# Performance work log

Measured on AMD Instinct MI355X. Metric: run time of the kernel, lower is better.

Reference implementation:

```python
import jax, jax.numpy as jnp
import numpy as np

BINS = 256

def _conv_x(t, k):
    # t: [N,1,H,W], k: [3] tap filter along width, 'same' padding
    return jax.lax.conv_general_dilated(t, k.reshape(1, 1, 1, 3), (1, 1), [(0, 0), (1, 1)])

def _conv_y(t, k):
    # t: [N,1,H,W], k: [3] tap filter along height, 'same' padding
    return jax.lax.conv_general_dilated(t, k.reshape(1, 1, 3, 1), (1, 1), [(1, 1), (0, 0)])

def calc_invCR(x):
    # Vectorized equivalent of the per-slice torch.histc loop:
    # 256-bin histogram over [-1,1] per (batch*channel) slice, Shannon entropy in bits / 8.
    n, _, h, w = x.shape
    res = h * w
    xf = x.reshape(n, res)
    valid = ((xf >= -1.0) & (xf <= 1.0)).astype(jnp.float32)
    # bin index; value exactly == max (1.0) falls into the last bin, matching torch.histc
    bins = jnp.clip(jnp.floor((xf + 1.0) * (BINS / 2.0)), 0, BINS - 1).astype(jnp.int32)
    counts = jnp.zeros((n, BINS), jnp.float32).at[jnp.arange(n)[:, None], bins].add(valid)
    p = counts / res
    ent = jnp.sum(jnp.where(p > 0, -p * jnp.log2(jnp.where(p > 0, p, 1.0)), 0.0))
    return ent / (8.0 * n)

def _forward(x, px, ux, cx, rx, py, uy, cy, ry):
    b, c, h, w = x.shape
    img = x.reshape(b * c, 1, h, w)
    cur = img
    xos, yos = [], []
    for lvl in range(5):
        xe, xo = cur[:, :, :, ::2], cur[:, :, :, 1::2]
        xo = xo - _conv_x(xe, px)
        xe = xe + _conv_x(xo, ux)
        xo = xo - _conv_x(xe, cx)
        xe = xe + _conv_x(xo, rx)
        ye, yo = xe[:, :, ::2, :], xe[:, :, 1::2, :]
        yo = yo - _conv_y(ye, py)
        if lvl < 2:
            ye = ye + _conv_y(yo, uy)
        # levels 3-5 in the source apply update_y to the (discarded) x?e tensor
        # (`x3e = x3e + self.update_y(x3o)`); that result is never used, so it is a
        # no-op for the output and is faithfully omitted here.
        yo = yo - _conv_y(ye, cy)
        ye = ye + _conv_y(yo, ry)
        xos.append(xo)
        yos.append(yo)
        cur = ye
    out = cur
    for xo, yo in zip(reversed(xos), reversed(yos)):
        out = jnp.concatenate((jnp.concatenate((out, yo), axis=2), xo), axis=3)
    deltas = jnp.fmod(out + 1.0, 2.0) - 1.0  # wrap residuals into [-1,1]
    loss1 = 255.0 * jnp.sqrt(jnp.mean(jnp.square(deltas)))
    loss0 = 255.0 * jnp.sqrt(jnp.mean(jnp.square(img)))
    invCR0 = calc_invCR(img)
    invCR1 = calc_invCR(deltas)
    return loss1, loss0, invCR0, invCR1

def setup_inputs() -> dict:
    key = jax.random.key(0)
    ks = jax.random.split(key, 9)
    inp = {"x": jax.random.uniform(ks[0], (32, 3, 512, 512), jnp.float32)}
    for i, name in enumerate(["px", "ux", "cx", "rx", "py", "uy", "cy", "ry"]):
        inp[name] = 0.25 * jax.random.normal(ks[i + 1], (3,), jnp.float32)
    return inp

def reference(x, px, ux, cx, rx, py, uy, cy, ry):
    return _forward(x, px, ux, cx, rx, py, uy, cy, ry)
```

## Files before the change

### kernel.cpp

```cpp
#include <hip/hip_runtime.h>
#include <math.h>

#define NIMG 96
#define NSLOT 1024
#define RES_INV (1.0f / 262144.0f)

__device__ __forceinline__ float wrap1(float v) {
  float t = v + 1.0f;
  return t - 2.0f * truncf(t * 0.5f) - 1.0f;
}
__device__ __forceinline__ int bin_fast(float v) {
  int b = (int)fmaf(v, 128.0f, 128.0f);
  return (b > 255) ? 255 : b;
}

template<int P, int SEGP, int USE_UY, int DO_IMG>
__global__ void __launch_bounds__(256) klift_fused(
    const float* __restrict__ src, float* __restrict__ ye_out,
    const float* __restrict__ kpx, const float* __restrict__ kux,
    const float* __restrict__ kcx, const float* __restrict__ krx,
    const float* __restrict__ kpy, const float* __restrict__ kuy,
    const float* __restrict__ kcy, const float* __restrict__ kry,
    double* __restrict__ partial,
    unsigned* __restrict__ hist_img, unsigned* __restrict__ hist_delta)
{
  constexpr int W2 = 64 * P;
  constexpr int H2 = W2;
  constexpr int H  = 2 * H2;
  constexpr int NP = SEGP + 8;
  constexpr int NR = 2 * NP;
  constexpr int NITER = NR / 4;
  __shared__ float tile[NR][W2];
  __shared__ unsigned shd[2][256];
  __shared__ unsigned shi[2][256];

  const int t = threadIdx.x, w = t >> 6, lane = t & 63;
  const int hsel = w >> 1;
  const int img = blockIdx.y;
  const int R0 = blockIdx.x * SEGP;
  const int base_in = 2 * R0 - 8;

  shd[0][t] = 0; shd[1][t] = 0;
  if (DO_IMG) { shi[0][t] = 0; shi[1][t] = 0; }
  __syncthreads();

  const float px0 = kpx[0], px1 = kpx[1], px2 = kpx[2];
  const float ux0 = kux[0], ux1 = kux[1], ux2 = kux[2];
  const float cx0 = kcx[0], cx1 = kcx[1], cx2 = kcx[2];
  const float rx0 = krx[0], rx1 = krx[1], rx2 = krx[2];
  const float py0 = kpy[0], py1 = kpy[1], py2 = kpy[2];
  const float uy0 = kuy[0], uy1 = kuy[1], uy2 = kuy[2];
  const float cy0 = kcy[0], cy1 = kcy[1], cy2 = kcy[2];
  const float ry0 = kry[0], ry1 = kry[1], ry2 = kry[2];

  const float* ip = src + (size_t)img * H * (2 * W2);
  float sqi = 0.f, sqd = 0.f;

  auto stepm = [&](float (&d)[P], float (&s)[P], float k0, float k1, float k2) {
    float L = __shfl_up(s[P - 1], 1); if (lane == 0) L = 0.f;
    float R = __shfl_down(s[0], 1);   if (lane == 63) R = 0.f;
    float prev = L;
#pragma unroll
    for (int j = 0; j < P; j++) {
      float nxt = (j == P - 1) ? R : s[(j + 1) < P ? (j + 1) : 0];
      d[j] = fmaf(k0, prev, fmaf(k1, s[j], fmaf(k2, nxt, d[j])));
      prev = s[j];
    }
  };
  auto ldrow = [&](int lr, float4& A, float4& B, bool chk) {
    const int gin = base_in + lr;
    if (!chk || ((unsigned)gin < (unsigned)H)) {
      const float* rp = ip + (size_t)gin * (2 * W2) + lane * (2 * P);
      if (P == 1) { float2 v = *(const float2*)rp; A.x = v.x; A.y = v.y; }
      else {
        A = *(const float4*)rp;
        if (P == 4) B = *(const float4*)(rp + 4);
      }
    } else {
      A = make_float4(0.f, 0.f, 0.f, 0.f);
      B = make_float4(0.f, 0.f, 0.f, 0.f);
    }
  };

  const int wcol = (P == 4) ? ((lane ^ ((lane >> 3) & 7)) * 4)
                 : (P == 2) ? (lane * 2) : lane;

  float4 cA = make_float4(0.f,0.f,0.f,0.f), cB = cA, nA = cA, nB = cA;
  ldrow(w, cA, cB, true);
#pragma unroll
  for (int i = 0; i < NITER; ++i) {
    const int lr = w + 4 * i;
    if (i + 1 < NITER)
      ldrow(lr + 4, nA, nB, (i + 1 < 2) || (i + 1 >= NITER - 2));
    const bool owned = (i >= 2) && (i < NITER - 2);
    float e[P], o[P];
    e[0] = cA.x; o[0] = cA.y;
    if (P >= 2) { e[P > 1 ? 1 : 0] = cA.z; o[P > 1 ? 1 : 0] = cA.w; }
    if (P == 4) {
      e[P > 2 ? 2 : 0] = cB.x; o[P > 2 ? 2 : 0] = cB.y;
      e[P > 3 ? 3 : 0] = cB.z; o[P > 3 ? 3 : 0] = cB.w;
    }
    if (DO_IMG && owned) {
#pragma unroll
      for (int j = 0; j < P; j++) {
        sqi += e[j] * e[j] + o[j] * o[j];
        atomicAdd(&shi[hsel][bin_fast(e[j])], 1u);
        atomicAdd(&shi[hsel][bin_fast(o[j])], 1u);
      }
    }
    stepm(o, e, -px0, -px1, -px2);
    stepm(e, o,  ux0,  ux1,  ux2);
    stepm(o, e, -cx0, -cx1, -cx2);
    stepm(e, o,  rx0,  rx1,  rx2);
    if (P == 4) {
      *(float4*)&tile[lr][wcol] =
          make_float4(e[0], e[P > 1 ? 1 : 0], e[P > 2 ? 2 : 0], e[P > 3 ? 3 : 0]);
    } else if (P == 2) {
      *(float2*)&tile[lr][wcol] = make_float2(e[0], e[P > 1 ? 1 : 0]);
    } else {
      tile[lr][wcol] = e[0];
    }
    if (owned) {
#pragma unroll
      for (int j = 0; j < P; j++) {
        float d = wrap1(o[j]);
        sqd += d * d;
        atomicAdd(&shd[hsel][bin_fast(d)], 1u);
      }
    }
    cA = nA; cB = nB;
  }
  __syncthreads();

  {
    constexpr int NSP = 256 / W2;
    constexpr int LEN = SEGP / NSP;
    constexpr int WIN = LEN + 8;
    const int col = t % W2;
    const int half = t / W2;
    const int q0 = half * LEN;
    int colr;
    if (P == 4) {
      const int ch = (col >> 2) ^ ((col >> 5) & 7);
      colr = (ch << 2) | (col & 3);
    } else colr = col;

    float ee[WIN], oo[WIN];
#pragma unroll
    for (int q = 0; q < WIN; ++q) {
      ee[q] = tile[2 * (q0 + q)][colr];
      oo[q] = tile[2 * (q0 + q) + 1][colr];
    }
#pragma unroll
    for (int q = 0; q < WIN; ++q) {
      float U = (q > 0) ? ee[q - 1] : 0.f;
      float D = (q < WIN - 1) ? ee[q + 1] : 0.f;
      oo[q] = fmaf(-py0, U, fmaf(-py1, ee[q], fmaf(-py2, D, oo[q])));
    }
    if (USE_UY) {
#pragma unroll
      for (int q = 0; q < WIN; ++q) {
        float U = (q > 0) ? oo[q - 1] : 0.f;
        float D = (q < WIN - 1) ? oo[q + 1] : 0.f;
        ee[q] = fmaf(uy0, U, fmaf(uy1, oo[q], fmaf(uy2, D, ee[q])));
      }
    }
#pragma unroll
    for (int q = 0; q < WIN; ++q) {
      float U = (q > 0) ? ee[q - 1] : 0.f;
      float D = (q < WIN - 1) ? ee[q + 1] : 0.f;
      oo[q] = fmaf(-cy0, U, fmaf(-cy1, ee[q], fmaf(-cy2, D, oo[q])));
    }
#pragma unroll
    for (int q = 0; q < WIN; ++q) {
      float U = (q > 0) ? oo[q - 1] : 0.f;
      float D = (q < WIN - 1) ? oo[q + 1] : 0.f;
      ee[q] = fmaf(ry0, U, fmaf(ry1, oo[q], fmaf(ry2, D, ee[q])));
    }
    float* outp = ye_out + (size_t)img * H2 * W2 + col;
#pragma unroll
    for (int q = 4; q < 4 + LEN; ++q) {
      const int g = R0 + q0 + q - 4;
      float d = wrap1(oo[q]);
      sqd += d * d;
      atomicAdd(&shd[hsel][bin_fast(d)], 1u);
      outp[(size_t)g * W2] = ee[q];
    }
  }

  for (int off = 32; off; off >>= 1) {
    sqd += __shfl_down(sqd, off);
    if (DO_IMG) sqi += __shfl_down(sqi, off);
  }
  if (lane == 0) {
    const int bid = blockIdx.x + blockIdx.y * gridDim.x;
    const int slot = (bid * 4 + w) & (NSLOT - 1);
    atomicAdd(&partial[NSLOT + slot], (double)sqd);
    if (DO_IMG) atomicAdd(&partial[slot], (double)sqi);
  }
  __syncthreads();
  unsigned hd = shd[0][t] + shd[1][t];
  if (hd) atomicAdd(&hist_delta[img * 256 + t], hd);
  if (DO_IMG) {
    unsigned hi = shi[0][t] + shi[1][t];
    if (hi) atomicAdd(&hist_img[img * 256 + t], hi);
  }
}

__global__ void __launch_bounds__(256) klift_tail64(
    const float* __restrict__ src,
    const float* __restrict__ kpx, const float* __restrict__ kux,
    const float* __restrict__ kcx, const float* __restrict__ krx,
    const float* __restrict__ kpy, const float* __restrict__ kcy,
    const float* __restrict__ kry,
    double* __restrict__ partial, unsigned* __restrict__ hist_delta)
{
  __shared__ float tile[64][65];
  __shared__ unsigned shd[256];
  const int t = threadIdx.x;
  const int img = blockIdx.x;
  shd[t] = 0;

  const float* sp = src + (size_t)img * 64 * 64;
  for (int idx = t; idx < 64 * 16; idx += 256) {
    const int r = idx >> 4, c4 = (idx & 15) << 2;
    float4 v = *(const float4*)(sp + r * 64 + c4);
    tile[r][c4] = v.x; tile[r][c4 + 1] = v.y;
    tile[r][c4 + 2] = v.z; tile[r][c4 + 3] = v.w;
  }
  const float px0 = kpx[0], px1 = kpx[1], px2 = kpx[2];
  const float ux0 = kux[0], ux1 = kux[1], ux2 = kux[2];
  const float cx0 = kcx[0], cx1 = kcx[1], cx2 = kcx[2];
  const float rx0 = krx[0], rx1 = krx[1], rx2 = krx[2];
  const float pc0 = kpy[0] + kcy[0], pc1 = kpy[1] + kcy[1], pc2 = kpy[2] + kcy[2];
  const float ry0 = kry[0], ry1 = kry[1], ry2 = kry[2];
  float sqd = 0.f;
  __syncthreads();

  for (int l = 0; l < 2; ++l) {
    const int s = 1 << l, n = 64 >> l, half = n >> 1;
    const int totx = n * half;

    for (int idx = t; idx < totx; idx += 256) {
      const int r = (idx / half) * s, c = idx % half;
      float L = (c > 0) ? tile[r][(2 * c - 2) * s] : 0.f;
      float M = tile[r][2 * c * s];
      float R = (c < half - 1) ? tile[r][(2 * c + 2) * s] : 0.f;
      tile[r][(2 * c + 1) * s] -= px0 * L + px1 * M + px2 * R;
    }
    __syncthreads();
    for (int idx = t; idx < totx; idx += 256) {
      const int r = (idx / half) * s, c = idx % half;
      float L = (c > 0) ? tile[r][(2 * c - 1) * s] : 0.f;
      float M = tile[r][(2 * c + 1) * s];
      float R = (c < half - 1) ? tile[r][(2 * c + 3) * s] : 0.f;
      tile[r][2 * c * s] += ux0 * L + ux1 * M + ux2 * R;
    }
    __syncthreads();
    for (int idx = t; idx < totx; idx += 256) {
      const int r = (idx / half) * s, c = idx % half;
      float L = (c > 0) ? tile[r][(2 * c - 2) * s] : 0.f;
      float M = tile[r][2 * c * s];
      float R = (c < half - 1) ? tile[r][(2 * c + 2) * s] : 0.f;
      tile[r][(2 * c + 1) * s] -= cx0 * L + cx1 * M + cx2 * R;
    }
    __syncthreads();
    for (int idx = t; idx < totx; idx += 256) {
      const int r = (idx / half) * s, c = idx % half;
      float L = (c > 0) ? tile[r][(2 * c - 1) * s] : 0.f;
      float M = tile[r][(2 * c + 1) * s];
      float R = (c < half - 1) ? tile[r][(2 * c + 3) * s] : 0.f;
      tile[r][2 * c * s] += rx0 * L + rx1 * M + rx2 * R;
    }
    __syncthreads();
    for (int idx = t; idx < totx; idx += 256) {
      const int r = (idx / half) * s, c = idx % half;
      float d = wrap1(tile[r][(2 * c + 1) * s]);
      sqd += d * d;
      atomicAdd(&shd[bin_fast(d)], 1u);
    }
    const int toty = half * half;
    for (int idx = t; idx < toty; idx += 256) {
      const int r = idx / half, j = idx % half, col = j * 2 * s;
      float U = (r > 0) ? tile[(2 * r - 2) * s][col] : 0.f;
      float M = tile[(2 * r) * s][col];
      float D = (r < half - 1) ? tile[(2 * r + 2) * s][col] : 0.f;
      tile[(2 * r + 1) * s][col] -= pc0 * U + pc1 * M + pc2 * D;
    }
    __syncthreads();
    for (int idx = t; idx < toty; idx += 256) {
      const int r = idx / half, j = idx % half, col = j * 2 * s;
      float U = (r > 0) ? tile[(2 * r - 1) * s][col] : 0.f;
      float M = tile[(2 * r + 1) * s][col];
      float D = (r < half - 1) ? tile[(2 * r + 3) * s][col] : 0.f;
      tile[(2 * r) * s][col] += ry0 * U + ry1 * M + ry2 * D;
    }
    __syncthreads();
    for (int idx = t; idx < toty; idx += 256) {
      const int r = idx / half, j = idx % half, col = j * 2 * s;
      float d = wrap1(tile[(2 * r + 1) * s][col]);
      sqd += d * d;
      atomicAdd(&shd[bin_fast(d)], 1u);
      if (l == 1) {
        float d2 = wrap1(tile[(2 * r) * s][col]);
        sqd += d2 * d2;
        atomicAdd(&shd[bin_fast(d2)], 1u);
      }
    }
    __syncthreads();
  }

  for (int off = 32; off; off >>= 1) sqd += __shfl_down(sqd, off);
  __shared__ float swv[4];
  if ((t & 63) == 0) swv[t >> 6] = sqd;
  __syncthreads();
  if (t == 0) {
    double tot = (double)swv[0] + swv[1] + swv[2] + swv[3];
    atomicAdd(&partial[NSLOT + (img & (NSLOT - 1))], tot);
  }
  unsigned hd = shd[t];
  if (hd) atomicAdd(&hist_delta[img * 256 + t], hd);
}

__global__ void __launch_bounds__(256) kfinal(
    const double* __restrict__ partial,
    const unsigned* __restrict__ hist_img,
    const unsigned* __restrict__ hist_delta,
    float* __restrict__ out)
{
  __shared__ double sI[256], sD[256], sPi[256], sPd[256];
  const int t = threadIdx.x;
  double entI = 0.0, entD = 0.0;
  for (int img = 0; img < NIMG; ++img) {
    unsigned ci = hist_img[img * 256 + t];
    if (ci) { float p = (float)ci * RES_INV; entI += (double)(-p * log2f(p)); }
    unsigned cd = hist_delta[img * 256 + t];
    if (cd) { float p = (float)cd * RES_INV; entD += (double)(-p * log2f(p)); }
  }
  double pi = 0.0, pd = 0.0;
  for (int s = t; s < NSLOT; s += 256) {
    pi += partial[s];
    pd += partial[NSLOT + s];
  }
  sI[t] = entI; sD[t] = entD; sPi[t] = pi; sPd[t] = pd;
  __syncthreads();
  for (int s = 128; s; s >>= 1) {
    if (t < s) {
      sI[t] += sI[t + s]; sD[t] += sD[t + s];
      sPi[t] += sPi[t + s]; sPd[t] += sPd[t + s];
    }
    __syncthreads();
  }
  if (t == 0) {
    const double tot = (double)NIMG * 262144.0;
    out[0] = (float)(255.0 * sqrt(sPd[0] / tot));
    out[1] = (float)(255.0 * sqrt(sPi[0] / tot));
    out[2] = (float)(sI[0] / (8.0 * NIMG));
    out[3] = (float)(sD[0] / (8.0 * NIMG));
  }
}

extern "C" void kernel_launch(void* const* d_in, const int* in_sizes, int n_in,
                              void* d_out, int out_size, void* d_ws, size_t ws_size,
                              hipStream_t stream)
{
  const float* x  = (const float*)d_in[0];
  const float* px = (const float*)d_in[1];
  const float* ux = (const float*)d_in[2];
  const float* cx = (const float*)d_in[3];
  const float* rx = (const float*)d_in[4];
  const float* py = (const float*)d_in[5];
  const float* uy = (const float*)d_in[6];
  const float* cy = (const float*)d_in[7];
  const float* ry = (const float*)d_in[8];
  float* out = (float*)d_out;

  char* ws = (char*)d_ws;
  double*   partial    = (double*)ws;
  unsigned* hist_img   = (unsigned*)(ws + 2 * NSLOT * 8);
  unsigned* hist_delta = (unsigned*)(ws + 2 * NSLOT * 8 + NIMG * 256 * 4);
  float* buf0 = (float*)(ws + (1 << 20));
  float* buf1 = (float*)(ws + (1 << 20) + ((size_t)32 << 20));
  float* buf2 = (float*)(ws + (1 << 20) + ((size_t)40 << 20));

  hipMemsetAsync(ws, 0, 2 * NSLOT * 8 + 2 * NIMG * 256 * 4, stream);

  klift_fused<4, 8, 1, 1><<<dim3(32, NIMG), 256, 0, stream>>>(
      x, buf0, px, ux, cx, rx, py, uy, cy, ry, partial, hist_img, hist_delta);
  klift_fused<2, 8, 1, 0><<<dim3(16, NIMG), 256, 0, stream>>>(
      buf0, buf1, px, ux, cx, rx, py, uy, cy, ry, partial, hist_img, hist_delta);
  klift_fused<1, 8, 0, 0><<<dim3(8, NIMG), 256, 0, stream>>>(
      buf1, buf2, px, ux, cx, rx, py, uy, cy, ry, partial, hist_img, hist_delta);
  klift_tail64<<<NIMG, 256, 0, stream>>>(buf2, px, ux, cx, rx, py, cy, ry,
                                         partial, hist_delta);
  kfinal<<<1, 256, 0, stream>>>(partial, hist_img, hist_delta, out);
}
```

Measured before the change: 89.30 us.

## Split fused lifting kernel into separate horizontal and vertical pass kernels

Each of the first three fused lifting levels is split into two kernels: one runs the horizontal lifting steps and writes the x-even result to global memory, the other reads it back and runs the vertical lifting steps. This drops the 8-row halo recompute and the LDS tile used in the fused version. In exchange it adds a full-resolution global write and read of the intermediate, and three extra kernel launches. Histogram shared arrays are also padded to 257 entries and split into two copies in the tail kernel to reduce atomic contention.

```diff
diff --git a/kernel.cpp b/kernel.cpp
--- a/kernel.cpp
+++ b/kernel.cpp
@@ -14,44 +14,33 @@
   return (b > 255) ? 255 : b;
 }
 
-template<int P, int SEGP, int USE_UY, int DO_IMG>
-__global__ void __launch_bounds__(256) klift_fused(
-    const float* __restrict__ src, float* __restrict__ ye_out,
+template<int P, int DO_IMG>
+__global__ void __launch_bounds__(256) kx(
+    const float* __restrict__ src, float* __restrict__ xe_out,
     const float* __restrict__ kpx, const float* __restrict__ kux,
     const float* __restrict__ kcx, const float* __restrict__ krx,
-    const float* __restrict__ kpy, const float* __restrict__ kuy,
-    const float* __restrict__ kcy, const float* __restrict__ kry,
     double* __restrict__ partial,
     unsigned* __restrict__ hist_img, unsigned* __restrict__ hist_delta)
 {
   constexpr int W2 = 64 * P;
-  constexpr int H2 = W2;
-  constexpr int H  = 2 * H2;
-  constexpr int NP = SEGP + 8;
-  constexpr int NR = 2 * NP;
-  constexpr int NITER = NR / 4;
-  __shared__ float tile[NR][W2];
-  __shared__ unsigned shd[2][256];
-  __shared__ unsigned shi[2][256];
+  constexpr int H  = 128 * P;
+  __shared__ unsigned shd[2][257];
+  __shared__ unsigned shi[2][257];
 
   const int t = threadIdx.x, w = t >> 6, lane = t & 63;
   const int hsel = w >> 1;
   const int img = blockIdx.y;
-  const int R0 = blockIdx.x * SEGP;
-  const int base_in = 2 * R0 - 8;
-
-  shd[0][t] = 0; shd[1][t] = 0;
-  if (DO_IMG) { shi[0][t] = 0; shi[1][t] = 0; }
+  const int r0 = blockIdx.x * 16 + w * 4;
+
+  for (int i = t; i < 2 * 257; i += 256) ((unsigned*)shd)[i] = 0;
+  if (DO_IMG)
+    for (int i = t; i < 2 * 257; i += 256) ((unsigned*)shi)[i] = 0;
   __syncthreads();
 
   const float px0 = kpx[0], px1 = kpx[1], px2 = kpx[2];
   const float ux0 = kux[0], ux1 = kux[1], ux2 = kux[2];
   const float cx0 = kcx[0], cx1 = kcx[1], cx2 = kcx[2];
   const float rx0 = krx[0], rx1 = krx[1], rx2 = krx[2];
-  const float py0 = kpy[0], py1 = kpy[1], py2 = kpy[2];
-  const float uy0 = kuy[0], uy1 = kuy[1], uy2 = kuy[2];
-  const float cy0 = kcy[0], cy1 = kcy[1], cy2 = kcy[2];
-  const float ry0 = kry[0], ry1 = kry[1], ry2 = kry[2];
 
   const float* ip = src + (size_t)img * H * (2 * W2);
   float sqi = 0.f, sqd = 0.f;
@@ -67,124 +56,53 @@
       prev = s[j];
     }
   };
-  auto ldrow = [&](int lr, float4& A, float4& B, bool chk) {
-    const int gin = base_in + lr;
-    if (!chk || ((unsigned)gin < (unsigned)H)) {
-      const float* rp = ip + (size_t)gin * (2 * W2) + lane * (2 * P);
-      if (P == 1) { float2 v = *(const float2*)rp; A.x = v.x; A.y = v.y; }
-      else {
-        A = *(const float4*)rp;
-        if (P == 4) B = *(const float4*)(rp + 4);
-      }
-    } else {
-      A = make_float4(0.f, 0.f, 0.f, 0.f);
-      B = make_float4(0.f, 0.f, 0.f, 0.f);
-    }
-  };
-
-  const int wcol = (P == 4) ? ((lane ^ ((lane >> 3) & 7)) * 4)
-                 : (P == 2) ? (lane * 2) : lane;
-
-  float4 cA = make_float4(0.f,0.f,0.f,0.f), cB = cA, nA = cA, nB = cA;
-  ldrow(w, cA, cB, true);
-#pragma unroll
-  for (int i = 0; i < NITER; ++i) {
-    const int lr = w + 4 * i;
-    if (i + 1 < NITER)
-      ldrow(lr + 4, nA, nB, (i + 1 < 2) || (i + 1 >= NITER - 2));
-    const bool owned = (i >= 2) && (i < NITER - 2);
+
+  float4 A[4], B[4];
+#pragma unroll
+  for (int j = 0; j < 4; ++j) {
+    const float* rp = ip + (size_t)(r0 + j) * (2 * W2) + lane * (2 * P);
+    if (P == 1) { float2 v = *(const float2*)rp; A[j].x = v.x; A[j].y = v.y; }
+    else {
+      A[j] = *(const float4*)rp;
+      if (P == 4) B[j] = *(const float4*)(rp + 4);
+    }
+  }
+
+#pragma unroll
+  for (int j = 0; j < 4; ++j) {
     float e[P], o[P];
-    e[0] = cA.x; o[0] = cA.y;
-    if (P >= 2) { e[P > 1 ? 1 : 0] = cA.z; o[P > 1 ? 1 : 0] = cA.w; }
+    e[0] = A[j].x; o[0] = A[j].y;
+    if (P >= 2) { e[P > 1 ? 1 : 0] = A[j].z; o[P > 1 ? 1 : 0] = A[j].w; }
     if (P == 4) {
-      e[P > 2 ? 2 : 0] = cB.x; o[P > 2 ? 2 : 0] = cB.y;
-      e[P > 3 ? 3 : 0] = cB.z; o[P > 3 ? 3 : 0] = cB.w;
-    }
-    if (DO_IMG && owned) {
-#pragma unroll
-      for (int j = 0; j < P; j++) {
-        sqi += e[j] * e[j] + o[j] * o[j];
-        atomicAdd(&shi[hsel][bin_fast(e[j])], 1u);
-        atomicAdd(&shi[hsel][bin_fast(o[j])], 1u);
+      e[P > 2 ? 2 : 0] = B[j].x; o[P > 2 ? 2 : 0] = B[j].y;
+      e[P > 3 ? 3 : 0] = B[j].z; o[P > 3 ? 3 : 0] = B[j].w;
+    }
+    if (DO_IMG) {
+#pragma unroll
+      for (int jj = 0; jj < P; jj++) {
+        sqi += e[jj] * e[jj] + o[jj] * o[jj];
+        atomicAdd(&shi[hsel][bin_fast(e[jj])], 1u);
+        atomicAdd(&shi[hsel][bin_fast(o[jj])], 1u);
       }
     }
     stepm(o, e, -px0, -px1, -px2);
     stepm(e, o,  ux0,  ux1,  ux2);
     stepm(o, e, -cx0, -cx1, -cx2);
     stepm(e, o,  rx0,  rx1,  rx2);
+    float* orow = xe_out + ((size_t)img * H + r0 + j) * W2;
     if (P == 4) {
-      *(float4*)&tile[lr][wcol] =
+      *(float4*)(orow + lane * 4) =
           make_float4(e[0], e[P > 1 ? 1 : 0], e[P > 2 ? 2 : 0], e[P > 3 ? 3 : 0]);
     } else if (P == 2) {
-      *(float2*)&tile[lr][wcol] = make_float2(e[0], e[P > 1 ? 1 : 0]);
+      *(float2*)(orow + lane * 2) = make_float2(e[0], e[P > 1 ? 1 : 0]);
     } else {
-      tile[lr][wcol] = e[0];
-    }
-    if (owned) {
-#pragma unroll
-      for (int j = 0; j < P; j++) {
-        float d = wrap1(o[j]);
-        sqd += d * d;
-        atomicAdd(&shd[hsel][bin_fast(d)], 1u);
-      }
-    }
-    cA = nA; cB = nB;
-  }
-  __syncthreads();
-
-  {
-    constexpr int NSP = 256 / W2;
-    constexpr int LEN = SEGP / NSP;
-    constexpr int WIN = LEN + 8;
-    const int col = t % W2;
-    const int half = t / W2;
-    const int q0 = half * LEN;
-    int colr;
-    if (P == 4) {
-      const int ch = (col >> 2) ^ ((col >> 5) & 7);
-      colr = (ch << 2) | (col & 3);
-    } else colr = col;
-
-    float ee[WIN], oo[WIN];
-#pragma unroll
-    for (int q = 0; q < WIN; ++q) {
-      ee[q] = tile[2 * (q0 + q)][colr];
-      oo[q] = tile[2 * (q0 + q) + 1][colr];
-    }
-#pragma unroll
-    for (int q = 0; q < WIN; ++q) {
-      float U = (q > 0) ? ee[q - 1] : 0.f;
-      float D = (q < WIN - 1) ? ee[q + 1] : 0.f;
-      oo[q] = fmaf(-py0, U, fmaf(-py1, ee[q], fmaf(-py2, D, oo[q])));
-    }
-    if (USE_UY) {
-#pragma unroll
-      for (int q = 0; q < WIN; ++q) {
-        float U = (q > 0) ? oo[q - 1] : 0.f;
-        float D = (q < WIN - 1) ? oo[q + 1] : 0.f;
-        ee[q] = fmaf(uy0, U, fmaf(uy1, oo[q], fmaf(uy2, D, ee[q])));
-      }
-    }
-#pragma unroll
-    for (int q = 0; q < WIN; ++q) {
-      float U = (q > 0) ? ee[q - 1] : 0.f;
-      float D = (q < WIN - 1) ? ee[q + 1] : 0.f;
-      oo[q] = fmaf(-cy0, U, fmaf(-cy1, ee[q], fmaf(-cy2, D, oo[q])));
-    }
-#pragma unroll
-    for (int q = 0; q < WIN; ++q) {
-      float U = (q > 0) ? oo[q - 1] : 0.f;
-      float D = (q < WIN - 1) ? oo[q + 1] : 0.f;
-      ee[q] = fmaf(ry0, U, fmaf(ry1, oo[q], fmaf(ry2, D, ee[q])));
-    }
-    float* outp = ye_out + (size_t)img * H2 * W2 + col;
-#pragma unroll
-    for (int q = 4; q < 4 + LEN; ++q) {
-      const int g = R0 + q0 + q - 4;
-      float d = wrap1(oo[q]);
+      orow[lane] = e[0];
+    }
+#pragma unroll
+    for (int jj = 0; jj < P; jj++) {
+      float d = wrap1(o[jj]);
       sqd += d * d;
       atomicAdd(&shd[hsel][bin_fast(d)], 1u);
-      outp[(size_t)g * W2] = ee[q];
     }
   }
 
@@ -205,6 +123,94 @@
     unsigned hi = shi[0][t] + shi[1][t];
     if (hi) atomicAdd(&hist_img[img * 256 + t], hi);
   }
+}
+
+template<int P, int USE_UY>
+__global__ void __launch_bounds__(256) ky(
+    const float* __restrict__ xe, float* __restrict__ ye_out,
+    const float* __restrict__ kpy, const float* __restrict__ kuy,
+    const float* __restrict__ kcy, const float* __restrict__ kry,
+    double* __restrict__ partial, unsigned* __restrict__ hist_delta)
+{
+  constexpr int W2 = 64 * P;
+  constexpr int H2 = W2;
+  constexpr int NSP = 256 / W2;
+  constexpr int SEG = 16, WIN = 24;
+  __shared__ unsigned shd[2][257];
+
+  const int t = threadIdx.x;
+  const int img = blockIdx.y;
+  const int col = t % W2;
+  const int half = t / W2;
+  const int r0 = (blockIdx.x * NSP + half) * SEG;
+  const int hsel = (t >> 7) & 1;
+
+  for (int i = t; i < 2 * 257; i += 256) ((unsigned*)shd)[i] = 0;
+  __syncthreads();
+
+  const float py0 = kpy[0], py1 = kpy[1], py2 = kpy[2];
+  const float uy0 = kuy[0], uy1 = kuy[1], uy2 = kuy[2];
+  const float cy0 = kcy[0], cy1 = kcy[1], cy2 = kcy[2];
+  const float ry0 = kry[0], ry1 = kry[1], ry2 = kry[2];
+
+  const float* xin = xe + (size_t)img * (2 * H2) * W2 + col;
+  float ee[WIN], oo[WIN];
+#pragma unroll
+  for (int q = 0; q < WIN; ++q) {
+    const int g = r0 + q - 4;
+    const int gc = (g < 0) ? 0 : ((g >= H2) ? (H2 - 1) : g);
+    float v0 = xin[(size_t)(2 * gc) * W2];
+    float v1 = xin[(size_t)(2 * gc) * W2 + W2];
+    const bool ok = (unsigned)g < (unsigned)H2;
+    ee[q] = ok ? v0 : 0.f;
+    oo[q] = ok ? v1 : 0.f;
+  }
+#pragma unroll
+  for (int q = 0; q < WIN; ++q) {
+    float U = (q > 0) ? ee[q - 1] : 0.f;
+    float D = (q < WIN - 1) ? ee[q + 1] : 0.f;
+    oo[q] = fmaf(-py0, U, fmaf(-py1, ee[q], fmaf(-py2, D, oo[q])));
+  }
+  if (USE_UY) {
+#pragma unroll
+    for (int q = 0; q < WIN; ++q) {
+      float U = (q > 0) ? oo[q - 1] : 0.f;
+      float D = (q < WIN - 1) ? oo[q + 1] : 0.f;
+      ee[q] = fmaf(uy0, U, fmaf(uy1, oo[q], fmaf(uy2, D, ee[q])));
+    }
+  }
+#pragma unroll
+  for (int q = 0; q < WIN; ++q) {
+    float U = (q > 0) ? ee[q - 1] : 0.f;
+    float D = (q < WIN - 1) ? ee[q + 1] : 0.f;
+    oo[q] = fmaf(-cy0, U, fmaf(-cy1, ee[q], fmaf(-cy2, D, oo[q])));
+  }
+#pragma unroll
+  for (int q = 0; q < WIN; ++q) {
+    float U = (q > 0) ? oo[q - 1] : 0.f;
+    float D = (q < WIN - 1) ? oo[q + 1] : 0.f;
+    ee[q] = fmaf(ry0, U, fmaf(ry1, oo[q], fmaf(ry2, D, ee[q])));
+  }
+
+  float sqd = 0.f;
+  float* outp = ye_out + (size_t)img * H2 * W2 + col;
+#pragma unroll
+  for (int q = 4; q < 4 + SEG; ++q) {
+    const int g = r0 + q - 4;
+    float d = wrap1(oo[q]);
+    sqd += d * d;
+    atomicAdd(&shd[hsel][bin_fast(d)], 1u);
+    outp[(size_t)g * W2] = ee[q];
+  }
+
+  for (int off = 32; off; off >>= 1) sqd += __shfl_down(sqd, off);
+  if ((t & 63) == 0) {
+    const int bid = blockIdx.x + blockIdx.y * gridDim.x;
+    atomicAdd(&partial[NSLOT + ((bid * 4 + (t >> 6)) & (NSLOT - 1))], (double)sqd);
+  }
+  __syncthreads();
+  unsigned hd = shd[0][t] + shd[1][t];
+  if (hd) atomicAdd(&hist_delta[img * 256 + t], hd);
 }
 
 __global__ void __launch_bounds__(256) klift_tail64(
@@ -216,10 +222,11 @@
     double* __restrict__ partial, unsigned* __restrict__ hist_delta)
 {
   __shared__ float tile[64][65];
-  __shared__ unsigned shd[256];
+  __shared__ unsigned shd[2][257];
   const int t = threadIdx.x;
   const int img = blockIdx.x;
-  shd[t] = 0;
+  const int cd = t & 1;
+  for (int i = t; i < 2 * 257; i += 256) ((unsigned*)shd)[i] = 0;
 
   const float* sp = src + (size_t)img * 64 * 64;
   for (int idx = t; idx < 64 * 16; idx += 256) {
@@ -277,7 +284,7 @@
       const int r = (idx / half) * s, c = idx % half;
       float d = wrap1(tile[r][(2 * c + 1) * s]);
       sqd += d * d;
-      atomicAdd(&shd[bin_fast(d)], 1u);
+      atomicAdd(&shd[cd][bin_fast(d)], 1u);
     }
     const int toty = half * half;
     for (int idx = t; idx < toty; idx += 256) {
@@ -300,11 +307,11 @@
       const int r = idx / half, j = idx % half, col = j * 2 * s;
       float d = wrap1(tile[(2 * r + 1) * s][col]);
       sqd += d * d;
-      atomicAdd(&shd[bin_fast(d)], 1u);
+      atomicAdd(&shd[cd][bin_fast(d)], 1u);
       if (l == 1) {
         float d2 = wrap1(tile[(2 * r) * s][col]);
         sqd += d2 * d2;
-        atomicAdd(&shd[bin_fast(d2)], 1u);
+        atomicAdd(&shd[cd][bin_fast(d2)], 1u);
       }
     }
     __syncthreads();
@@ -318,7 +325,7 @@
     double tot = (double)swv[0] + swv[1] + swv[2] + swv[3];
     atomicAdd(&partial[NSLOT + (img & (NSLOT - 1))], tot);
   }
-  unsigned hd = shd[t];
+  unsigned hd = shd[0][t] + shd[1][t];
   if (hd) atomicAdd(&hist_delta[img * 256 + t], hd);
 }
 
@@ -379,19 +386,26 @@
   double*   partial    = (double*)ws;
   unsigned* hist_img   = (unsigned*)(ws + 2 * NSLOT * 8);
   unsigned* hist_delta = (unsigned*)(ws + 2 * NSLOT * 8 + NIMG * 256 * 4);
-  float* buf0 = (float*)(ws + (1 << 20));
-  float* buf1 = (float*)(ws + (1 << 20) + ((size_t)32 << 20));
-  float* buf2 = (float*)(ws + (1 << 20) + ((size_t)40 << 20));
+  float* bxe  = (float*)(ws + ((size_t)1 << 20));
+  float* bye0 = (float*)(ws + ((size_t)50 << 20));
+  float* bye1 = (float*)(ws + ((size_t)76 << 20));
+  float* bye2 = (float*)(ws + ((size_t)83 << 20));
 
   hipMemsetAsync(ws, 0, 2 * NSLOT * 8 + 2 * NIMG * 256 * 4, stream);
 
-  klift_fused<4, 8, 1, 1><<<dim3(32, NIMG), 256, 0, stream>>>(
-      x, buf0, px, ux, cx, rx, py, uy, cy, ry, partial, hist_img, hist_delta);
-  klift_fused<2, 8, 1, 0><<<dim3(16, NIMG), 256, 0, stream>>>(
-      buf0, buf1, px, ux, cx, rx, py, uy, cy, ry, partial, hist_img, hist_delta);
-  klift_fused<1, 8, 0, 0><<<dim3(8, NIMG), 256, 0, stream>>>(
-      buf1, buf2, px, ux, cx, rx, py, uy, cy, ry, partial, hist_img, hist_delta);
-  klift_tail64<<<NIMG, 256, 0, stream>>>(buf2, px, ux, cx, rx, py, cy, ry,
+  kx<4, 1><<<dim3(32, NIMG), 256, 0, stream>>>(
+      x, bxe, px, ux, cx, rx, partial, hist_img, hist_delta);
+  ky<4, 1><<<dim3(16, NIMG), 256, 0, stream>>>(
+      bxe, bye0, py, uy, cy, ry, partial, hist_delta);
+  kx<2, 0><<<dim3(16, NIMG), 256, 0, stream>>>(
+      bye0, bxe, px, ux, cx, rx, partial, hist_img, hist_delta);
+  ky<2, 1><<<dim3(4, NIMG), 256, 0, stream>>>(
+      bxe, bye1, py, uy, cy, ry, partial, hist_delta);
+  kx<1, 0><<<dim3(8, NIMG), 256, 0, stream>>>(
+      bye1, bxe, px, ux, cx, rx, partial, hist_img, hist_delta);
+  ky<1, 0><<<dim3(1, NIMG), 256, 0, stream>>>(
+      bxe, bye2, py, uy, cy, ry, partial, hist_delta);
+  klift_tail64<<<NIMG, 256, 0, stream>>>(bye2, px, ux, cx, rx, py, cy, ry,
                                          partial, hist_delta);
   kfinal<<<1, 256, 0, stream>>>(partial, hist_img, hist_delta, out);
 }
```

New measurement: 98.64 us. 10.5% more time.
